# Kernel tuning notes

Hardware: AMD Instinct MI355X
Metric: run time of the kernel (lower is better)

## Reference

```python
import jax, jax.numpy as jnp
import numpy as np

B, S_IMG, S_TXT, P, D, HEADS, HD = 1, 2048, 512, 4, 3072, 24, 128


def rmsnorm(x, weight=None, eps=1e-6):
    var = jnp.mean(jnp.square(x), axis=-1, keepdims=True)
    y = x * jax.lax.rsqrt(var + eps)
    return y * weight if weight is not None else y


def apply_rope(x, cos, sin):
    # x: [B,H,S,Dh]; cos/sin: [S,Dh]; interleaved real/imag rotation (diffusers use_real_unbind_dim=-1)
    xr = x.reshape(*x.shape[:-1], -1, 2)
    rot = jnp.stack([-xr[..., 1], xr[..., 0]], axis=-1).reshape(x.shape)
    return x * cos[None, None] + rot * sin[None, None]


def sdpa(q, k, v):
    scores = jnp.einsum('bhqd,bhkd->bhqk', q, k) / jnp.sqrt(jnp.asarray(q.shape[-1], q.dtype))
    return jnp.einsum('bhqk,bhkd->bhqd', jax.nn.softmax(scores, axis=-1), v)


def heads_split(x):
    # [B,S,D] -> [B,H,S,Dh]
    return x.reshape(x.shape[0], x.shape[1], HEADS, HD).transpose(0, 2, 1, 3)


def heads_merge(x):
    # [B,H,S,Dh] -> [B,S,D]
    return x.transpose(0, 2, 1, 3).reshape(x.shape[0], x.shape[2], HEADS * HD)


def setup_inputs() -> dict:
    key = jax.random.key(0)
    ks = jax.random.split(key, 32)
    init = lambda k, shape: (jax.random.normal(k, shape, dtype=jnp.float32) * 0.02)
    inp = {
        'hidden_states': jax.random.normal(ks[0], (B, S_IMG, D), dtype=jnp.float32),
        'encoder_hidden_states': jax.random.normal(ks[1], (B, S_TXT, D), dtype=jnp.float32),
        'ip_encoder_hidden_states': jax.random.normal(ks[2], (B, P, D), dtype=jnp.float32),
        'layer_scale': jax.random.uniform(ks[3], (B,), dtype=jnp.float32),
        'Wq': init(ks[4], (D, D)), 'bq': jnp.zeros((D,), jnp.float32),
        'Wk': init(ks[5], (D, D)), 'bk': jnp.zeros((D,), jnp.float32),
        'Wv': init(ks[6], (D, D)), 'bv': jnp.zeros((D,), jnp.float32),
        'norm_q_w': jnp.ones((HD,), jnp.float32),
        'norm_k_w': jnp.ones((HD,), jnp.float32),
        'Waq': init(ks[7], (D, D)), 'baq': jnp.zeros((D,), jnp.float32),
        'Wak': init(ks[8], (D, D)), 'bak': jnp.zeros((D,), jnp.float32),
        'Wav': init(ks[9], (D, D)), 'bav': jnp.zeros((D,), jnp.float32),
        'norm_aq_w': jnp.ones((HD,), jnp.float32),
        'norm_ak_w': jnp.ones((HD,), jnp.float32),
        'Wk_ip': init(ks[10], (D, D)),
        'Wv_ip': init(ks[11], (D, D)),
        'Wo': init(ks[12], (D, D)), 'bo': jnp.zeros((D,), jnp.float32),
        'Wao': init(ks[13], (D, D)), 'bao': jnp.zeros((D,), jnp.float32),
    }
    # rotary cos/sin over the joint (text+image) sequence, interleaved freqs per diffusers FLUX
    pos = jnp.arange(S_TXT + S_IMG, dtype=jnp.float32)
    inv_freq = 1.0 / (10000.0 ** (jnp.arange(0, HD, 2, dtype=jnp.float32) / HD))
    angles = pos[:, None] * inv_freq[None, :]            # [S, HD/2]
    angles = jnp.repeat(angles, 2, axis=-1)              # [S, HD]
    inp['cos'] = jnp.cos(angles)
    inp['sin'] = jnp.sin(angles)
    return inp


IP_SCALE = 1.0  # self.scale


def reference(hidden_states, encoder_hidden_states, ip_encoder_hidden_states, cos, sin,
              layer_scale, Wq, bq, Wk, bk, Wv, bv, norm_q_w, norm_k_w,
              Waq, baq, Wak, bak, Wav, bav, norm_aq_w, norm_ak_w,
              Wk_ip, Wv_ip, Wo, bo, Wao, bao):
    # image-stream projections
    q = heads_split(hidden_states @ Wq.T + bq)
    k = heads_split(hidden_states @ Wk.T + bk)
    v = heads_split(hidden_states @ Wv.T + bv)
    q = rmsnorm(q, norm_q_w, 1e-6)
    k = rmsnorm(k, norm_k_w, 1e-6)

    # IP-adapter cross-attention (queries = image tokens, kv = IP tokens)
    ip_k = rmsnorm(heads_split(ip_encoder_hidden_states @ Wk_ip.T), None, 1e-5)
    ip_v = heads_split(ip_encoder_hidden_states @ Wv_ip.T)
    ip_out = heads_merge(sdpa(q, ip_k, ip_v))            # [B, S_img, D]

    # text (encoder) stream projections, prepended to joint sequence
    eq = rmsnorm(heads_split(encoder_hidden_states @ Waq.T + baq), norm_aq_w, 1e-6)
    ek = rmsnorm(heads_split(encoder_hidden_states @ Wak.T + bak), norm_ak_w, 1e-6)
    ev = heads_split(encoder_hidden_states @ Wav.T + bav)
    q = jnp.concatenate([eq, q], axis=2)
    k = jnp.concatenate([ek, k], axis=2)
    v = jnp.concatenate([ev, v], axis=2)

    q = apply_rope(q, cos, sin)
    k = apply_rope(k, cos, sin)

    out = heads_merge(sdpa(q, k, v))                     # [B, S_txt+S_img, D]
    n_txt = encoder_hidden_states.shape[1]
    enc_out, img_out = out[:, :n_txt], out[:, n_txt:]

    ls = layer_scale.reshape(-1, 1, 1)
    img_out = img_out + IP_SCALE * ls * ip_out
    img_out = img_out @ Wo.T + bo
    enc_out = enc_out @ Wao.T + bao
    return (img_out, enc_out)
```

## Files before the change

### kernel.cpp

```cpp
#include <hip/hip_runtime.h>

typedef _Float16 half_t;
typedef _Float16 half2v __attribute__((ext_vector_type(2)));
typedef _Float16 half4v __attribute__((ext_vector_type(4)));
typedef _Float16 half8v __attribute__((ext_vector_type(8)));
typedef float    float4v __attribute__((ext_vector_type(4)));
typedef short    short8v __attribute__((ext_vector_type(8)));

#define S_IMG 2048
#define S_TXT 512
#define S_TOT 2560
#define NH    24
#define HD    128
#define DM    3072

__device__ __forceinline__ void gload16(const void* g, void* l) {
  __builtin_amdgcn_global_load_lds(
      (const __attribute__((address_space(1))) unsigned int*)g,
      (__attribute__((address_space(3))) unsigned int*)l, 16, 0, 0);
}

__global__ void cvt_kernel(const float* __restrict__ s, half_t* __restrict__ d, int n) {
  int i = (blockIdx.x * 256 + threadIdx.x) * 4;
  int stride = gridDim.x * 256 * 4;
  for (; i < n; i += stride) {
    float4v v = *(const float4v*)(s + i);
    half4v h;
    h[0] = (half_t)v[0]; h[1] = (half_t)v[1]; h[2] = (half_t)v[2]; h[3] = (half_t)v[3];
    *(half4v*)(d + i) = h;
  }
}

__global__ void cvt3_kernel(const float* __restrict__ s0, const float* __restrict__ s1,
                            const float* __restrict__ s2,
                            half_t* __restrict__ d0, half_t* __restrict__ d1,
                            half_t* __restrict__ d2, int n) {
  const float* s = blockIdx.y == 0 ? s0 : (blockIdx.y == 1 ? s1 : s2);
  half_t* d = blockIdx.y == 0 ? d0 : (blockIdx.y == 1 ? d1 : d2);
  int i = (blockIdx.x * 256 + threadIdx.x) * 8;
  int stride = gridDim.x * 256 * 8;
  for (; i < n; i += stride) {
    float4v v0 = *(const float4v*)(s + i);
    float4v v1 = *(const float4v*)(s + i + 4);
    half8v h;
    h[0] = (half_t)v0[0]; h[1] = (half_t)v0[1]; h[2] = (half_t)v0[2]; h[3] = (half_t)v0[3];
    h[4] = (half_t)v1[0]; h[5] = (half_t)v1[1]; h[6] = (half_t)v1[2]; h[7] = (half_t)v1[3];
    *(half8v*)(d + i) = h;
  }
}

template <typename OUT>
__device__ __forceinline__ void gemm_tile(half_t* As, half_t* Bs,
                                          const half_t* __restrict__ A,
                                          const half_t* __restrict__ Bt,
                                          const float* __restrict__ bias,
                                          OUT* __restrict__ C, int bm, int bn) {
  const int K = DM, N = DM;
  const int tid = threadIdx.x, wid = tid >> 6, l = tid & 63;
  const int wm = (wid >> 1) * 64, wn = (wid & 1) * 64;
  const int l15 = l & 15, l4 = l >> 4;
  float4v acc[4][4] = {};

  const half_t* ga = A + (long)(bm + wid * 32 + (l >> 2)) * K + (l & 3) * 8;
  const half_t* gb = Bt + (long)(bn + wid * 32 + (l >> 2)) * K + (l & 3) * 8;
  char* lAs = (char*)As + wid * 2048;
  char* lBs = (char*)Bs + wid * 2048;
  const long rowstep = 16l * K;

  for (int k0 = 0; k0 < K; k0 += 32) {
    gload16(ga + k0, lAs);
    gload16(ga + rowstep + k0, lAs + 1024);
    gload16(gb + k0, lBs);
    gload16(gb + rowstep + k0, lBs + 1024);
    __syncthreads();
    half8v af[4], bf[4];
#pragma unroll
    for (int i = 0; i < 4; i++) af[i] = *(const half8v*)&As[(wm + i * 16 + l15) * 32 + l4 * 8];
#pragma unroll
    for (int j = 0; j < 4; j++) bf[j] = *(const half8v*)&Bs[(wn + j * 16 + l15) * 32 + l4 * 8];
#pragma unroll
    for (int i = 0; i < 4; i++)
#pragma unroll
      for (int j = 0; j < 4; j++)
        acc[i][j] = __builtin_amdgcn_mfma_f32_16x16x32_f16(af[i], bf[j], acc[i][j], 0, 0, 0);
    __syncthreads();
  }
#pragma unroll
  for (int i = 0; i < 4; i++)
#pragma unroll
    for (int j = 0; j < 4; j++) {
      int row = bm + wm + i * 16 + l4 * 4;
      int col = bn + wn + j * 16 + l15;
      float bv = bias ? bias[col] : 0.0f;
#pragma unroll
      for (int r = 0; r < 4; r++) {
        float v = acc[i][j][r] + bv;
        C[(long)(row + r) * N + col] = (OUT)v;
      }
    }
}

template <int NROW>
__global__ __launch_bounds__(256) void gemm3_kernel(const half_t* __restrict__ A,
                                                    const half_t* __restrict__ W0,
                                                    const half_t* __restrict__ W1,
                                                    const half_t* __restrict__ W2,
                                                    const float* b0, const float* b1, const float* b2,
                                                    half_t* O0, half_t* O1, half_t* O2) {
  __shared__ half_t As[128 * 32];
  __shared__ half_t Bs[128 * 32];
  int b = blockIdx.x;
  int q = (72 * NROW) >> 3;
  int wg = (b & 7) * q + (b >> 3);
  int col = wg / NROW, row = wg % NROW;
  int sel = col / 24;
  const half_t* Bt = sel == 0 ? W0 : (sel == 1 ? W1 : W2);
  const float* bias = sel == 0 ? b0 : (sel == 1 ? b1 : b2);
  half_t* C = sel == 0 ? O0 : (sel == 1 ? O1 : O2);
  gemm_tile<half_t>(As, Bs, A, Bt, bias, C, row * 128, (col % 24) * 128);
}

__global__ __launch_bounds__(256) void gemm_out_kernel(const half_t* __restrict__ ocomb,
                                                       const half_t* __restrict__ Wo_h,
                                                       const half_t* __restrict__ Wao_h,
                                                       const float* bo, const float* bao,
                                                       float* out_img, float* out_enc) {
  __shared__ half_t As[128 * 32];
  __shared__ half_t Bs[128 * 32];
  int b = blockIdx.x;
  int wg = (b & 7) * 60 + (b >> 3);
  int col = wg / 20, r = wg % 20;
  bool enc = r >= 16;
  const half_t* A = enc ? ocomb : ocomb + (long)S_TXT * DM;
  int bm = (enc ? (r - 16) : r) * 128;
  gemm_tile<float>(As, Bs, A, enc ? Wao_h : Wo_h, enc ? bao : bo,
                   enc ? out_enc : out_img, bm, col * 128);
}

__global__ __launch_bounds__(256) void ip_proj_kernel(const float* __restrict__ x,
                                                      const float* __restrict__ W,
                                                      float* __restrict__ out) {
  int n = blockIdx.x * 4 + (threadIdx.x >> 6);
  int l = threadIdx.x & 63;
  const float* wr = W + (long)n * DM;
  float acc[4] = {0.f, 0.f, 0.f, 0.f};
  for (int k = l * 4; k < DM; k += 256) {
    float4v wv = *(const float4v*)(wr + k);
#pragma unroll
    for (int p = 0; p < 4; p++) {
      float4v xv = *(const float4v*)(x + p * DM + k);
      acc[p] += wv[0] * xv[0] + wv[1] * xv[1] + wv[2] * xv[2] + wv[3] * xv[3];
    }
  }
#pragma unroll
  for (int off = 32; off; off >>= 1)
#pragma unroll
    for (int p = 0; p < 4; p++) acc[p] += __shfl_xor(acc[p], off, 64);
  if (l == 0)
#pragma unroll
    for (int p = 0; p < 4; p++) out[p * DM + n] = acc[p];
}

__global__ void ip_norm_kernel(const float* __restrict__ kr, const float* __restrict__ vr,
                               half_t* __restrict__ kh, half_t* __restrict__ vh) {
  int t = blockIdx.x;
  int l = threadIdx.x;
  int d = l * 2;
  if (t < 96) {
    int base = (t / 24) * DM + (t % 24) * HD;
    float x0 = kr[base + d], x1 = kr[base + d + 1];
    float ss = x0 * x0 + x1 * x1;
#pragma unroll
    for (int off = 32; off; off >>= 1) ss += __shfl_xor(ss, off, 64);
    float r = rsqrtf(ss * (1.0f / HD) + 1e-5f);
    kh[base + d] = (half_t)(x0 * r);
    kh[base + d + 1] = (half_t)(x1 * r);
  } else {
    int t2 = t - 96;
    int base = (t2 / 24) * DM + (t2 % 24) * HD;
    vh[base + d] = (half_t)vr[base + d];
    vh[base + d + 1] = (half_t)vr[base + d + 1];
  }
}

__global__ __launch_bounds__(256) void prep_kernel(
    const half_t* __restrict__ qraw, const half_t* __restrict__ kraw,
    const half_t* __restrict__ eq, const half_t* __restrict__ ek,
    const float* __restrict__ nqw, const float* __restrict__ nkw,
    const float* __restrict__ naqw, const float* __restrict__ nakw,
    const float* __restrict__ cosb, const float* __restrict__ sinb,
    half_t* __restrict__ qcat, half_t* __restrict__ kcat, half_t* __restrict__ qnr) {
  int task = blockIdx.x * 4 + (threadIdx.x >> 6);
  int l = threadIdx.x & 63;
  int s = task / NH, h = task - (task / NH) * NH;
  int d = l * 2;
  const half_t *qs, *ks;
  const float *wq, *wk;
  if (s < S_TXT) {
    long base = (long)s * DM + h * HD;
    qs = eq + base; ks = ek + base;
    wq = naqw; wk = nakw;
  } else {
    long base = (long)(s - S_TXT) * DM + h * HD;
    qs = qraw + base; ks = kraw + base;
    wq = nqw; wk = nkw;
  }
  half2v qv = *(const half2v*)(qs + d);
  half2v kv = *(const half2v*)(ks + d);
  float q0 = (float)qv[0], q1 = (float)qv[1];
  float k0 = (float)kv[0], k1 = (float)kv[1];
  float ssq = q0 * q0 + q1 * q1;
  float ssk = k0 * k0 + k1 * k1;
#pragma unroll
  for (int off = 32; off; off >>= 1) {
    ssq += __shfl_xor(ssq, off, 64);
    ssk += __shfl_xor(ssk, off, 64);
  }
  float rq = rsqrtf(ssq * (1.0f / HD) + 1e-6f);
  float rk = rsqrtf(ssk * (1.0f / HD) + 1e-6f);
  float qn0 = q0 * rq * wq[d], qn1 = q1 * rq * wq[d + 1];
  float kn0 = k0 * rk * wk[d], kn1 = k1 * rk * wk[d + 1];
  if (s >= S_TXT) {
    half2v o; o[0] = (half_t)qn0; o[1] = (half_t)qn1;
    *(half2v*)(qnr + ((long)h * S_IMG + (s - S_TXT)) * HD + d) = o;
  }
  float c0 = cosb[s * HD + d], c1 = cosb[s * HD + d + 1];
  float s0 = sinb[s * HD + d], s1 = sinb[s * HD + d + 1];
  float qo0 = qn0 * c0 - qn1 * s0, qo1 = qn1 * c1 + qn0 * s1;
  float ko0 = kn0 * c0 - kn1 * s0, ko1 = kn1 * c1 + kn0 * s1;
  long ci = ((long)h * S_TOT + s) * HD + d;
  half2v oq; oq[0] = (half_t)qo0; oq[1] = (half_t)qo1;
  half2v ok; ok[0] = (half_t)ko0; ok[1] = (half_t)ko1;
  *(half2v*)(qcat + ci) = oq;
  *(half2v*)(kcat + ci) = ok;
}

__global__ __launch_bounds__(256) void vtrans_kernel(const half_t* __restrict__ ev,
                                                     const half_t* __restrict__ vraw,
                                                     half_t* __restrict__ vcatT) {
  __shared__ half_t T[64][136];
  int h = blockIdx.y, sb = blockIdx.x * 64;
  int t = threadIdx.x;
#pragma unroll
  for (int i = 0; i < 4; i++) {
    int c = t + i * 256;
    int row = c >> 4, col = (c & 15) * 8;
    int s = sb + row;
    const half_t* src = (s < S_TXT) ? ev + (long)s * DM + h * HD + col
                                    : vraw + (long)(s - S_TXT) * DM + h * HD + col;
    *(half8v*)&T[row][col] = *(const half8v*)src;
  }
  __syncthreads();
#pragma unroll
  for (int i = 0; i < 4; i++) {
    int c = t + i * 256;
    int d = c >> 3, sc = (c & 7) * 8;
    half8v v;
#pragma unroll
    for (int j = 0; j < 8; j++) v[j] = T[sc + j][d];
    *(half8v*)(vcatT + ((long)h * HD + d) * S_TOT + sb + sc) = v;
  }
}

__global__ __launch_bounds__(256) void ip_attn_kernel(const half_t* __restrict__ qnr,
                                                      const half_t* __restrict__ kh,
                                                      const half_t* __restrict__ vh,
                                                      half_t* __restrict__ ipout) {
  int task = blockIdx.x * 4 + (threadIdx.x >> 6);
  int l = threadIdx.x & 63;
  int h = task >> 11;
  int s = task & 2047;
  int d = l * 2;
  half2v qv = *(const half2v*)(qnr + ((long)h * S_IMG + s) * HD + d);
  float q0 = (float)qv[0], q1 = (float)qv[1];
  float sc[4];
#pragma unroll
  for (int p = 0; p < 4; p++) {
    half2v kv = *(const half2v*)(kh + p * DM + h * HD + d);
    sc[p] = q0 * (float)kv[0] + q1 * (float)kv[1];
  }
#pragma unroll
  for (int off = 32; off; off >>= 1)
#pragma unroll
    for (int p = 0; p < 4; p++) sc[p] += __shfl_xor(sc[p], off, 64);
  float m = fmaxf(fmaxf(sc[0], sc[1]), fmaxf(sc[2], sc[3]));
  float e[4], sum = 0.f;
#pragma unroll
  for (int p = 0; p < 4; p++) { e[p] = __expf((sc[p] - m) * 0.088388347648318447f); sum += e[p]; }
  float inv = 1.0f / sum;
  float o0 = 0.f, o1 = 0.f;
#pragma unroll
  for (int p = 0; p < 4; p++) {
    half2v vv = *(const half2v*)(vh + p * DM + h * HD + d);
    o0 += e[p] * (float)vv[0];
    o1 += e[p] * (float)vv[1];
  }
  o0 *= inv; o1 *= inv;
  half2v ov; ov[0] = (half_t)o0; ov[1] = (half_t)o1;
  *(half2v*)(ipout + (long)s * DM + h * HD + d) = ov;
}

__global__ __launch_bounds__(256, 2) void flash_kernel(const half_t* __restrict__ qcat,
                                                       const half_t* __restrict__ kcat,
                                                       const half_t* __restrict__ vcatT,
                                                       const half_t* __restrict__ ipout,
                                                       const float* __restrict__ lsp,
                                                       half_t* __restrict__ ocomb) {
  __shared__ half_t Ks[3 * 32 * 128];
  __shared__ half_t Vs[3 * 128 * 32];
  __shared__ half_t Pw[4][32 * 40];
  int b = blockIdx.x;
  int wg = (b & 7) * 60 + (b >> 3);
  const int h = wg / 20, qb = wg % 20;
  const int tid = threadIdx.x, wid = tid >> 6, l = tid & 63;
  const int l15 = l & 15, l4 = l >> 4;
  const float CEXP = 0.12754137969983614f;

  half8v qf[2][4];
#pragma unroll
  for (int t = 0; t < 2; t++) {
    int qrow = qb * 128 + wid * 32 + t * 16 + l15;
    const half_t* qp = qcat + ((long)h * S_TOT + qrow) * HD;
#pragma unroll
    for (int kk = 0; kk < 4; kk++) qf[t][kk] = *(const half8v*)(qp + kk * 32 + l4 * 8);
  }
  float4v o[2][8] = {};
  float mreg[2] = {-3.0e38f, -3.0e38f};
  float lreg[2] = {0.f, 0.f};
  const float ls = lsp[0];

  const char* kb = (const char*)(kcat + (long)h * S_TOT * HD);
  const char* vb = (const char*)(vcatT + (long)h * HD * S_TOT);
  int kof[2];
  long vof[2];
#pragma unroll
  for (int c = 0; c < 2; c++) {
    int L = wid * 2048 + c * 1024 + l * 16;
    kof[c] = L ^ (((L >> 8) & 7) << 4);
    vof[c] = (long)(L >> 6) * (S_TOT * 2) + (L & 63);
  }

#define STAGE(KT, SEL)                                                        \
  {                                                                           \
    char* kd = (char*)Ks + (SEL) * 8192 + wid * 2048;                         \
    char* vd = (char*)Vs + (SEL) * 8192 + wid * 2048;                         \
    _Pragma("unroll") for (int c = 0; c < 2; c++) {                           \
      gload16(kb + (long)(KT) * 256 + kof[c], kd + c * 1024);                 \
      gload16(vb + vof[c] + (KT) * 2, vd + c * 1024);                         \
    }                                                                         \
  }

  STAGE(0, 0);
  STAGE(32, 1);

  const int NT = S_TOT / 32;
  for (int it = 0; it < NT; it++) {
    int cur = it % 3;
    if (it + 1 < NT) asm volatile("s_waitcnt vmcnt(4)" ::: "memory");
    else             asm volatile("s_waitcnt vmcnt(0)" ::: "memory");
    __builtin_amdgcn_s_barrier();
    __builtin_amdgcn_sched_barrier(0);
    if (it + 2 < NT) STAGE((it + 2) * 32, (it + 2) % 3);

    const char* KsB = (const char*)Ks + cur * 8192;
    const char* VsB = (const char*)Vs + cur * 8192;

    float4v s0[2] = {}, s1[2] = {};
    __builtin_amdgcn_s_setprio(1);
#pragma unroll
    for (int nb = 0; nb < 2; nb++) {
      int krow = nb * 16 + l15;
      int rb = krow << 8;
      int sw = (krow & 7) << 4;
#pragma unroll
      for (int kk = 0; kk < 4; kk++) {
        half8v kf = *(const half8v*)(KsB + rb + ((kk * 64 + l4 * 16) ^ sw));
        s0[nb] = __builtin_amdgcn_mfma_f32_16x16x32_f16(kf, qf[0][kk], s0[nb], 0, 0, 0);
        s1[nb] = __builtin_amdgcn_mfma_f32_16x16x32_f16(kf, qf[1][kk], s1[nb], 0, 0, 0);
      }
    }
    __builtin_amdgcn_s_setprio(0);
#pragma unroll
    for (int t = 0; t < 2; t++) {
      float4v* st = t ? s1 : s0;
      float mt = fmaxf(fmaxf(fmaxf(st[0][0], st[0][1]), fmaxf(st[0][2], st[0][3])),
                       fmaxf(fmaxf(st[1][0], st[1][1]), fmaxf(st[1][2], st[1][3])));
      mt = fmaxf(mt, __shfl_xor(mt, 16, 64));
      mt = fmaxf(mt, __shfl_xor(mt, 32, 64));
      if (__any((mt - mreg[t]) * CEXP > 8.0f)) {
        float mn = fmaxf(mreg[t], mt);
        float alv = exp2f((mreg[t] - mn) * CEXP);
        mreg[t] = mn;
        lreg[t] *= alv;
#pragma unroll
        for (int r = 0; r < 4; r++) {
          float ar = __shfl(alv, l4 * 4 + r, 64);
#pragma unroll
          for (int cb = 0; cb < 8; cb++) o[t][cb][r] *= ar;
        }
      }
      float sum = 0.f;
#pragma unroll
      for (int nb = 0; nb < 2; nb++) {
        half4v ph;
#pragma unroll
        for (int r = 0; r < 4; r++) {
          float e = exp2f((st[nb][r] - mreg[t]) * CEXP);
          sum += e;
          ph[r] = (half_t)e;
        }
        *(half4v*)&Pw[wid][(t * 16 + l15) * 40 + nb * 16 + l4 * 4] = ph;
      }
      sum += __shfl_xor(sum, 16, 64);
      sum += __shfl_xor(sum, 32, 64);
      lreg[t] += sum;
    }
    half8v pa0 = *(const half8v*)&Pw[wid][l15 * 40 + l4 * 8];
    half8v pa1 = *(const half8v*)&Pw[wid][(16 + l15) * 40 + l4 * 8];
    __builtin_amdgcn_s_setprio(1);
#pragma unroll
    for (int cb = 0; cb < 8; cb++) {
      int row = cb * 16 + l15;
      half8v vf = *(const half8v*)(VsB + row * 64 + l4 * 16);
      o[0][cb] = __builtin_amdgcn_mfma_f32_16x16x32_f16(pa0, vf, o[0][cb], 0, 0, 0);
      o[1][cb] = __builtin_amdgcn_mfma_f32_16x16x32_f16(pa1, vf, o[1][cb], 0, 0, 0);
    }
    __builtin_amdgcn_s_setprio(0);
  }
#undef STAGE
#pragma unroll
  for (int t = 0; t < 2; t++) {
    float invq = 1.0f / lreg[t];
#pragma unroll
    for (int r = 0; r < 4; r++) {
      float inv = __shfl(invq, l4 * 4 + r, 64);
      int s = qb * 128 + wid * 32 + t * 16 + l4 * 4 + r;
#pragma unroll
      for (int cb = 0; cb < 8; cb++) {
        int col = h * HD + cb * 16 + l15;
        float val = o[t][cb][r] * inv;
        if (s >= S_TXT) val += ls * (float)ipout[(long)(s - S_TXT) * DM + col];
        ocomb[(long)s * DM + col] = (half_t)val;
      }
    }
  }
}

extern "C" void kernel_launch(void* const* d_in, const int* in_sizes, int n_in,
                              void* d_out, int out_size, void* d_ws, size_t ws_size,
                              hipStream_t stream) {
  (void)in_sizes; (void)n_in; (void)out_size; (void)ws_size;
  const float* hs    = (const float*)d_in[0];
  const float* enc   = (const float*)d_in[1];
  const float* ipenc = (const float*)d_in[2];
  const float* lsc   = (const float*)d_in[3];
  const float* Wq  = (const float*)d_in[4];  const float* bq  = (const float*)d_in[5];
  const float* Wk  = (const float*)d_in[6];  const float* bk  = (const float*)d_in[7];
  const float* Wv  = (const float*)d_in[8];  const float* bv  = (const float*)d_in[9];
  const float* nqw = (const float*)d_in[10]; const float* nkw = (const float*)d_in[11];
  const float* Waq = (const float*)d_in[12]; const float* baq = (const float*)d_in[13];
  const float* Wak = (const float*)d_in[14]; const float* bak = (const float*)d_in[15];
  const float* Wav = (const float*)d_in[16]; const float* bav = (const float*)d_in[17];
  const float* naqw= (const float*)d_in[18]; const float* nakw= (const float*)d_in[19];
  const float* Wkip= (const float*)d_in[20]; const float* Wvip= (const float*)d_in[21];
  const float* Wo  = (const float*)d_in[22]; const float* bo  = (const float*)d_in[23];
  const float* Wao = (const float*)d_in[24]; const float* bao = (const float*)d_in[25];
  const float* cosb= (const float*)d_in[26]; const float* sinb= (const float*)d_in[27];

  const size_t WSZ = (size_t)DM * DM;
  const size_t HSZ = (size_t)S_IMG * DM;
  const size_t ESZ = (size_t)S_TXT * DM;
  const size_t CSZ = (size_t)NH * S_TOT * HD;

  half_t* base = (half_t*)d_ws;
  half_t* W3    = base;
  half_t* hs_h  = W3 + 3 * WSZ;
  half_t* enc_h = hs_h + HSZ;
  half_t* qkvr  = enc_h + ESZ;
  half_t* eqkv  = qkvr + 3 * HSZ;
  half_t* qcat  = eqkv + 3 * ESZ;
  half_t* kcat  = qcat + CSZ;
  half_t* vcatT = kcat + CSZ;

  half_t* q_raw = qkvr;
  half_t* k_raw = qkvr + HSZ;
  half_t* v_raw = qkvr + 2 * HSZ;
  half_t* eq_r  = eqkv;
  half_t* ek_r  = eqkv + ESZ;
  half_t* ev_r  = eqkv + 2 * ESZ;
  half_t* qnr   = hs_h;
  half_t* ipout = qkvr;
  half_t* ocomb = qkvr + HSZ;
  float*  ipk_raw = (float*)enc_h;
  float*  ipv_raw = ipk_raw + 4 * DM;
  half_t* ipk_h  = enc_h + 16 * DM;
  half_t* ipv_h  = ipk_h + 4 * DM;

  cvt_kernel<<<1024, 256, 0, stream>>>(hs, hs_h, (int)HSZ);
  cvt_kernel<<<512, 256, 0, stream>>>(enc, enc_h, (int)ESZ);

  cvt3_kernel<<<dim3(1024, 3), 256, 0, stream>>>(Wq, Wk, Wv, W3, W3 + WSZ, W3 + 2 * WSZ, (int)WSZ);
  gemm3_kernel<16><<<1152, 256, 0, stream>>>(hs_h, W3, W3 + WSZ, W3 + 2 * WSZ,
                                             bq, bk, bv, q_raw, k_raw, v_raw);
  cvt3_kernel<<<dim3(1024, 3), 256, 0, stream>>>(Waq, Wak, Wav, W3, W3 + WSZ, W3 + 2 * WSZ, (int)WSZ);
  gemm3_kernel<4><<<288, 256, 0, stream>>>(enc_h, W3, W3 + WSZ, W3 + 2 * WSZ,
                                           baq, bak, bav, eq_r, ek_r, ev_r);
  ip_proj_kernel<<<768, 256, 0, stream>>>(ipenc, Wkip, ipk_raw);
  ip_proj_kernel<<<768, 256, 0, stream>>>(ipenc, Wvip, ipv_raw);
  ip_norm_kernel<<<192, 64, 0, stream>>>(ipk_raw, ipv_raw, ipk_h, ipv_h);

  prep_kernel<<<(S_TOT * NH) / 4, 256, 0, stream>>>(q_raw, k_raw, eq_r, ek_r,
                                                    nqw, nkw, naqw, nakw, cosb, sinb,
                                                    qcat, kcat, qnr);
  vtrans_kernel<<<dim3(S_TOT / 64, NH), 256, 0, stream>>>(ev_r, v_raw, vcatT);

  ip_attn_kernel<<<(NH * S_IMG) / 4, 256, 0, stream>>>(qnr, ipk_h, ipv_h, ipout);

  flash_kernel<<<480, 256, 0, stream>>>(qcat, kcat, vcatT, ipout, lsc, ocomb);

  float* out_img = (float*)d_out;
  float* out_enc = (float*)d_out + (size_t)S_IMG * DM;
  cvt3_kernel<<<dim3(1024, 2), 256, 0, stream>>>(Wo, Wao, Wao, W3, W3 + WSZ, W3 + 2 * WSZ, (int)WSZ);
  gemm_out_kernel<<<480, 256, 0, stream>>>(ocomb, W3, W3 + WSZ, bo, bao, out_img, out_enc);
}
```

Measured before the change: 607.7 us.

## Triple-buffer GEMM LDS loads with swizzle, vectorize IP attention, swizzle flash V reads

The GEMM tile loop now uses a three-stage LDS ring with asynchronous global-to-LDS loads and vmcnt-based waits. This replaces the two full __syncthreads per k-step and lets loads overlap the MFMAs. A/B tiles and the flash kernel's V tile get an XOR swizzle on the column offset to reduce LDS bank conflicts. The IP attention kernel handles 16 tokens per block with 8-wide half loads and 16-lane reductions instead of 2-wide loads and 64-lane shuffles. LDS use per GEMM block triples, which may reduce occupancy.

```diff
diff --git a/kernel.cpp b/kernel.cpp
--- a/kernel.cpp
+++ b/kernel.cpp
@@ -61,30 +61,53 @@
   const int l15 = l & 15, l4 = l >> 4;
   float4v acc[4][4] = {};
 
-  const half_t* ga = A + (long)(bm + wid * 32 + (l >> 2)) * K + (l & 3) * 8;
-  const half_t* gb = Bt + (long)(bn + wid * 32 + (l >> 2)) * K + (l & 3) * 8;
-  char* lAs = (char*)As + wid * 2048;
-  char* lBs = (char*)Bs + wid * 2048;
+  const int scol = ((l & 3) ^ ((l >> 3) & 3)) * 8;
+  const half_t* ga = A + (long)(bm + wid * 32 + (l >> 2)) * K + scol;
+  const half_t* gb = Bt + (long)(bn + wid * 32 + (l >> 2)) * K + scol;
   const long rowstep = 16l * K;
 
-  for (int k0 = 0; k0 < K; k0 += 32) {
-    gload16(ga + k0, lAs);
-    gload16(ga + rowstep + k0, lAs + 1024);
-    gload16(gb + k0, lBs);
-    gload16(gb + rowstep + k0, lBs + 1024);
-    __syncthreads();
+#define GSTAGE(T, SEL)                                                        \
+  {                                                                           \
+    char* a_d = (char*)As + (SEL) * 8192 + wid * 2048;                        \
+    char* b_d = (char*)Bs + (SEL) * 8192 + wid * 2048;                        \
+    int k0 = (T) * 32;                                                        \
+    gload16(ga + k0, a_d);                                                    \
+    gload16(ga + rowstep + k0, a_d + 1024);                                   \
+    gload16(gb + k0, b_d);                                                    \
+    gload16(gb + rowstep + k0, b_d + 1024);                                   \
+  }
+
+  GSTAGE(0, 0);
+  GSTAGE(1, 1);
+
+  const int NT = K / 32;
+  const int cofs = (l4 * 16) ^ (((l15 >> 1) & 3) << 4);
+  for (int t = 0; t < NT; t++) {
+    int cur = t % 3;
+    if (t + 1 < NT) asm volatile("s_waitcnt vmcnt(4)" ::: "memory");
+    else            asm volatile("s_waitcnt vmcnt(0)" ::: "memory");
+    __builtin_amdgcn_s_barrier();
+    __builtin_amdgcn_sched_barrier(0);
+    if (t + 2 < NT) GSTAGE(t + 2, (t + 2) % 3);
+    __builtin_amdgcn_sched_barrier(0);
+    const char* AsB = (const char*)As + cur * 8192;
+    const char* BsB = (const char*)Bs + cur * 8192;
     half8v af[4], bf[4];
 #pragma unroll
-    for (int i = 0; i < 4; i++) af[i] = *(const half8v*)&As[(wm + i * 16 + l15) * 32 + l4 * 8];
-#pragma unroll
-    for (int j = 0; j < 4; j++) bf[j] = *(const half8v*)&Bs[(wn + j * 16 + l15) * 32 + l4 * 8];
+    for (int i = 0; i < 4; i++)
+      af[i] = *(const half8v*)(AsB + (wm + i * 16 + l15) * 64 + cofs);
+#pragma unroll
+    for (int j = 0; j < 4; j++)
+      bf[j] = *(const half8v*)(BsB + (wn + j * 16 + l15) * 64 + cofs);
+    __builtin_amdgcn_s_setprio(1);
 #pragma unroll
     for (int i = 0; i < 4; i++)
 #pragma unroll
       for (int j = 0; j < 4; j++)
         acc[i][j] = __builtin_amdgcn_mfma_f32_16x16x32_f16(af[i], bf[j], acc[i][j], 0, 0, 0);
-    __syncthreads();
-  }
+    __builtin_amdgcn_s_setprio(0);
+  }
+#undef GSTAGE
 #pragma unroll
   for (int i = 0; i < 4; i++)
 #pragma unroll
@@ -107,8 +130,8 @@
                                                     const half_t* __restrict__ W2,
                                                     const float* b0, const float* b1, const float* b2,
                                                     half_t* O0, half_t* O1, half_t* O2) {
-  __shared__ half_t As[128 * 32];
-  __shared__ half_t Bs[128 * 32];
+  __shared__ half_t As[3 * 128 * 32];
+  __shared__ half_t Bs[3 * 128 * 32];
   int b = blockIdx.x;
   int q = (72 * NROW) >> 3;
   int wg = (b & 7) * q + (b >> 3);
@@ -125,8 +148,8 @@
                                                        const half_t* __restrict__ Wao_h,
                                                        const float* bo, const float* bao,
                                                        float* out_img, float* out_enc) {
-  __shared__ half_t As[128 * 32];
-  __shared__ half_t Bs[128 * 32];
+  __shared__ half_t As[3 * 128 * 32];
+  __shared__ half_t Bs[3 * 128 * 32];
   int b = blockIdx.x;
   int wg = (b & 7) * 60 + (b >> 3);
   int col = wg / 20, r = wg % 20;
@@ -266,38 +289,42 @@
                                                       const half_t* __restrict__ kh,
                                                       const half_t* __restrict__ vh,
                                                       half_t* __restrict__ ipout) {
-  int task = blockIdx.x * 4 + (threadIdx.x >> 6);
-  int l = threadIdx.x & 63;
+  int tid = threadIdx.x;
+  int task = blockIdx.x * 16 + (tid >> 4);
+  int l16 = tid & 15;
   int h = task >> 11;
   int s = task & 2047;
-  int d = l * 2;
-  half2v qv = *(const half2v*)(qnr + ((long)h * S_IMG + s) * HD + d);
-  float q0 = (float)qv[0], q1 = (float)qv[1];
+  int d = l16 * 8;
+  half8v qv = *(const half8v*)(qnr + ((long)h * S_IMG + s) * HD + d);
   float sc[4];
 #pragma unroll
   for (int p = 0; p < 4; p++) {
-    half2v kv = *(const half2v*)(kh + p * DM + h * HD + d);
-    sc[p] = q0 * (float)kv[0] + q1 * (float)kv[1];
-  }
-#pragma unroll
-  for (int off = 32; off; off >>= 1)
-#pragma unroll
-    for (int p = 0; p < 4; p++) sc[p] += __shfl_xor(sc[p], off, 64);
+    half8v kv = *(const half8v*)(kh + p * DM + h * HD + d);
+    float a = 0.f;
+#pragma unroll
+    for (int j = 0; j < 8; j++) a += (float)qv[j] * (float)kv[j];
+    sc[p] = a;
+  }
+#pragma unroll
+  for (int off = 8; off; off >>= 1)
+#pragma unroll
+    for (int p = 0; p < 4; p++) sc[p] += __shfl_xor(sc[p], off, 16);
   float m = fmaxf(fmaxf(sc[0], sc[1]), fmaxf(sc[2], sc[3]));
   float e[4], sum = 0.f;
 #pragma unroll
   for (int p = 0; p < 4; p++) { e[p] = __expf((sc[p] - m) * 0.088388347648318447f); sum += e[p]; }
   float inv = 1.0f / sum;
-  float o0 = 0.f, o1 = 0.f;
+  float o[8] = {};
 #pragma unroll
   for (int p = 0; p < 4; p++) {
-    half2v vv = *(const half2v*)(vh + p * DM + h * HD + d);
-    o0 += e[p] * (float)vv[0];
-    o1 += e[p] * (float)vv[1];
-  }
-  o0 *= inv; o1 *= inv;
-  half2v ov; ov[0] = (half_t)o0; ov[1] = (half_t)o1;
-  *(half2v*)(ipout + (long)s * DM + h * HD + d) = ov;
+    half8v vv = *(const half8v*)(vh + p * DM + h * HD + d);
+#pragma unroll
+    for (int j = 0; j < 8; j++) o[j] += e[p] * (float)vv[j];
+  }
+  half8v ov;
+#pragma unroll
+  for (int j = 0; j < 8; j++) ov[j] = (half_t)(o[j] * inv);
+  *(half8v*)(ipout + (long)s * DM + h * HD + d) = ov;
 }
 
 __global__ __launch_bounds__(256, 2) void flash_kernel(const half_t* __restrict__ qcat,
@@ -337,7 +364,8 @@
   for (int c = 0; c < 2; c++) {
     int L = wid * 2048 + c * 1024 + l * 16;
     kof[c] = L ^ (((L >> 8) & 7) << 4);
-    vof[c] = (long)(L >> 6) * (S_TOT * 2) + (L & 63);
+    int vrow = L >> 6;
+    vof[c] = (long)vrow * (S_TOT * 2) + ((L & 63) ^ (((vrow >> 1) & 3) << 4));
   }
 
 #define STAGE(KT, SEL)                                                        \
@@ -354,6 +382,7 @@
   STAGE(32, 1);
 
   const int NT = S_TOT / 32;
+  const int vofs = (l4 * 16) ^ (((l15 >> 1) & 3) << 4);
   for (int it = 0; it < NT; it++) {
     int cur = it % 3;
     if (it + 1 < NT) asm volatile("s_waitcnt vmcnt(4)" ::: "memory");
@@ -421,7 +450,7 @@
 #pragma unroll
     for (int cb = 0; cb < 8; cb++) {
       int row = cb * 16 + l15;
-      half8v vf = *(const half8v*)(VsB + row * 64 + l4 * 16);
+      half8v vf = *(const half8v*)(VsB + row * 64 + vofs);
       o[0][cb] = __builtin_amdgcn_mfma_f32_16x16x32_f16(pa0, vf, o[0][cb], 0, 0, 0);
       o[1][cb] = __builtin_amdgcn_mfma_f32_16x16x32_f16(pa1, vf, o[1][cb], 0, 0, 0);
     }
@@ -514,7 +543,7 @@
                                                     qcat, kcat, qnr);
   vtrans_kernel<<<dim3(S_TOT / 64, NH), 256, 0, stream>>>(ev_r, v_raw, vcatT);
 
-  ip_attn_kernel<<<(NH * S_IMG) / 4, 256, 0, stream>>>(qnr, ipk_h, ipv_h, ipout);
+  ip_attn_kernel<<<(NH * S_IMG) / 16, 256, 0, stream>>>(qnr, ipk_h, ipv_h, ipout);
 
   flash_kernel<<<480, 256, 0, stream>>>(qcat, kcat, vcatT, ipout, lsc, ocomb);
 
```

New measurement: 600.0 us. No clear change (-1.3%).
